# Optimization experiments

Hardware: AMD Instinct MI355X
Metric: run time of the kernel (lower is better)

## Reference

```python
import jax, jax.numpy as jnp
import numpy as np

RES = 128
RANK = 8
PE_L = 6
ENC = 256
N = 1 << 20
IN_DIM = RANK + 3 + 3 * 2 * PE_L  # 47


def _linear_init(key, fan_in, fan_out):
    kw, kb = jax.random.split(key)
    bound = 1.0 / np.sqrt(fan_in)
    W = jax.random.uniform(kw, (fan_in, fan_out), jnp.float32, -bound, bound)
    b = jax.random.uniform(kb, (fan_out,), jnp.float32, -bound, bound)
    return W, b


def setup_inputs() -> dict:
    key = jax.random.key(0)
    ks = jax.random.split(key, 12)
    x = jax.random.uniform(ks[0], (N, 3), jnp.float32, -1.0, 1.0)
    f_xy = jax.random.normal(ks[1], (RANK, RES, RES), jnp.float32)
    f_xz = jax.random.normal(ks[2], (RANK, RES, RES), jnp.float32)
    f_yz = jax.random.normal(ks[3], (RANK, RES, RES), jnp.float32)
    W0, b0 = _linear_init(ks[4], IN_DIM, ENC)
    W1, b1 = _linear_init(ks[5], ENC, ENC)
    W2, b2 = _linear_init(ks[6], ENC, ENC)
    W3, b3 = _linear_init(ks[7], ENC, ENC)
    W_sig, b_sig = _linear_init(ks[8], ENC, 1)
    W_rgb, b_rgb = _linear_init(ks[9], ENC, 3)
    return {
        "x": x, "f_xy": f_xy, "f_xz": f_xz, "f_yz": f_yz,
        "W0": W0, "b0": b0, "W1": W1, "b1": b1,
        "W2": W2, "b2": b2, "W3": W3, "b3": b3,
        "W_sig": W_sig, "b_sig": b_sig, "W_rgb": W_rgb, "b_rgb": b_rgb,
    }


def reference(x, f_xy, f_xz, f_yz, W0, b0, W1, b1, W2, b2, W3, b3,
              W_sig, b_sig, W_rgb, b_rgb):
    # map [-1,1] coords to voxel indices (truncation like .long(), then clamp)
    coords = (x + 1.0) * 0.5 * (RES - 1)
    idx = jnp.clip(coords.astype(jnp.int32), 0, RES - 1)
    ix, iy, iz = idx[:, 0], idx[:, 1], idx[:, 2]
    # tri-planar CP-factor gathers: each [rank, N]
    feat = (f_xy[:, iy, ix] + f_xz[:, iz, ix] + f_yz[:, iz, iy]).T  # [N, rank]
    # positional encoding: [x, (sin(2^l x), cos(2^l x)) for l in 0..L-1]
    freqs = 2.0 ** jnp.arange(PE_L, dtype=jnp.float32)          # [L]
    ang = x[:, None, :] * freqs[None, :, None]                   # [N, L, 3]
    pe_sc = jnp.concatenate([jnp.sin(ang), jnp.cos(ang)], axis=-1)  # [N, L, 6]
    pe = jnp.concatenate([x, pe_sc.reshape(x.shape[0], -1)], axis=-1)  # [N, 3+6L]
    h = jnp.concatenate([feat, pe], axis=-1)                     # [N, 47]
    for W, b in ((W0, b0), (W1, b1), (W2, b2), (W3, b3)):
        h = jax.nn.relu(h @ W + b)
    sigma = jax.nn.softplus(h @ W_sig + b_sig)                   # [N, 1]
    rgb = jax.nn.sigmoid(h @ W_rgb + b_rgb)                      # [N, 3]
    return (rgb, sigma)
```

## Files before the change

kernel.cpp:

```cpp
#include <hip/hip_runtime.h>
#include <hip/hip_bf16.h>

typedef unsigned short ushort_t;
typedef unsigned int uint_t;
typedef unsigned char uchar_t;

typedef float f32x4 __attribute__((ext_vector_type(4)));
typedef float f32x16 __attribute__((ext_vector_type(16)));
typedef int v8i __attribute__((ext_vector_type(8)));

#define NPTS (1 << 20)

#define OFF_FLAG 0
#define OFF_B0   16
#define OFF_B1   272
#define OFF_B2   528
#define OFF_B3   784
#define OFF_BSIG 1040
#define OFF_BRGB 1041
#define OFF_W0   1056
#define OFF_W1   9248
#define OFF_W2   42016
#define OFF_W3   74784
#define OFF_WH   107552
#define OFF_PL   111648

__device__ __forceinline__ float bf2f(ushort_t u) {
  union { uint_t i; float f; } c; c.i = ((uint_t)u) << 16; return c.f;
}
__device__ __forceinline__ ushort_t f2bf(float f) {
  union { float f; uint_t i; } c; c.f = f;
  uint_t x = c.i;
  return (ushort_t)((x + 0x7fffu + ((x >> 16) & 1u)) >> 16);
}
__device__ __forceinline__ uint_t f2fp8b_soft(float x) {
  union { float f; uint_t u; } v; v.f = x;
  uint_t s = (v.u >> 24) & 0x80u;
  float ax = fabsf(x);
  if (ax < 0.015625f) return s | (uint_t)(int)rintf(ax * 512.0f);
  if (ax >= 448.0f) return s | 0x7Eu;
  int e2; float m = frexpf(ax, &e2);
  int q = (int)rintf(m * 16.0f) - 8;
  int e = e2 - 1;
  if (q == 8) { q = 0; ++e; }
  if (e == 8 && q > 6) q = 6;
  return s | ((uint_t)(e + 7) << 3) | (uint_t)q;
}

#if defined(__has_builtin)
#if __has_builtin(__builtin_amdgcn_cvt_pk_fp8_f32)
#define HAVE_HW_FP8 1
#endif
#if __has_builtin(__builtin_amdgcn_mfma_scale_f32_32x32x64_f8f6f4)
#define HAVE_MX 1
#endif
#endif

#ifdef HAVE_HW_FP8
__device__ __forceinline__ uint_t pk4fp8(float a, float b, float c, float d) {
  uint_t r = (uint_t)__builtin_amdgcn_cvt_pk_fp8_f32(a, b, 0, false);
  r = (uint_t)__builtin_amdgcn_cvt_pk_fp8_f32(c, d, r, true);
  return r;
}
__device__ __forceinline__ uchar_t f2fp8(float x) {
  return (uchar_t)(__builtin_amdgcn_cvt_pk_fp8_f32(x, 0.0f, 0, false) & 0xFFu);
}
#else
__device__ __forceinline__ uint_t pk4fp8(float a, float b, float c, float d) {
  return f2fp8b_soft(a) | (f2fp8b_soft(b) << 8) | (f2fp8b_soft(c) << 16) | (f2fp8b_soft(d) << 24);
}
__device__ __forceinline__ uchar_t f2fp8(float x) { return (uchar_t)f2fp8b_soft(x); }
#endif

union AU { v8i v; uint2 u2[4]; long l[4]; };

__device__ __forceinline__ f32x16 mx_mfma(const AU& A, const AU& B, f32x16 C) {
#ifdef HAVE_MX
  return __builtin_amdgcn_mfma_scale_f32_32x32x64_f8f6f4(
      A.v, B.v, C, 0, 0, 0, (int)0x7F7F7F7F, 0, (int)0x7F7F7F7F);
#else
#pragma unroll
  for (int s = 0; s < 4; ++s)
    C = __builtin_amdgcn_mfma_f32_32x32x16_fp8_fp8(A.l[s], B.l[s], C, 0, 0, 0);
  return C;
#endif
}

__device__ __forceinline__ float ldf(const void* p, long i, int isbf) {
  return isbf ? bf2f(((const ushort_t*)p)[i]) : ((const float*)p)[i];
}
__device__ __forceinline__ ushort_t ldbf(const void* p, long i, int isbf) {
  return isbf ? ((const ushort_t*)p)[i] : f2bf(((const float*)p)[i]);
}
__device__ __forceinline__ void stf(void* p, long i, int isbf, float v) {
  if (isbf) ((ushort_t*)p)[i] = f2bf(v);
  else      ((float*)p)[i] = v;
}

__device__ __forceinline__ int fp8addr(int p, int k) {
  return ((p >> 5) << 13) + ((k >> 4) << 9) + (((k >> 3) & 1) << 8)
       + ((p & 31) << 3) + (k & 7);
}

__global__ void sniff_dtype(const void* __restrict__ f, ushort_t* __restrict__ ws) {
  __shared__ int s_cnt;
  if (threadIdx.x == 0) s_cnt = 0;
  __syncthreads();
  const ushort_t* u = (const ushort_t*)f;
  int c = 0;
  for (int j = 0; j < 4; ++j) {
    ushort_t v = u[(threadIdx.x * 4 + j) * 2];
    int e = (v >> 7) & 0xFF;
    if (e > 100 && e < 140) ++c;
  }
  atomicAdd(&s_cnt, c);
  __syncthreads();
  if (threadIdx.x == 0) ((uint_t*)ws)[0] = (s_cnt >= 160) ? 1u : 0u;
}

__global__ void prep_bias(const void* __restrict__ b0, const void* __restrict__ b1,
                          const void* __restrict__ b2, const void* __restrict__ b3,
                          const void* __restrict__ bsig, const void* __restrict__ brgb,
                          ushort_t* __restrict__ ws) {
  const int isbf = (int)((const uint_t*)ws)[0];
  int i = threadIdx.x;
  ws[OFF_B0 + i] = ldbf(b0, i, isbf);
  ws[OFF_B1 + i] = ldbf(b1, i, isbf);
  ws[OFF_B2 + i] = ldbf(b2, i, isbf);
  ws[OFF_B3 + i] = ldbf(b3, i, isbf);
  if (i == 0) ws[OFF_BSIG] = ldbf(bsig, 0, isbf);
  if (i < 3) ws[OFF_BRGB + i] = ldbf(brgb, i, isbf);
}

__global__ void prep_weights(const void* __restrict__ W0,
                             const void* __restrict__ W1,
                             const void* __restrict__ W2,
                             const void* __restrict__ W3,
                             const void* __restrict__ Wsig,
                             const void* __restrict__ Wrgb,
                             ushort_t* __restrict__ ws) {
  const int isbf = (int)((const uint_t*)ws)[0];
  int t = blockIdx.x * 256 + threadIdx.x;
  if (t >= 432 * 64) return;
  int lane = t & 63;
  int tile = t >> 6;
  const void* src = nullptr;
  ushort_t* dst;
  int local, Ksrc = 256;
  bool head = false;
  if (tile < 32) { local = tile; src = W0; Ksrc = 47; dst = ws + OFF_W0 + (size_t)local * 256; }
  else if (tile < 160) { local = tile - 32;  src = W1; dst = ws + OFF_W1 + (size_t)local * 256; }
  else if (tile < 288) { local = tile - 160; src = W2; dst = ws + OFF_W2 + (size_t)local * 256; }
  else if (tile < 416) { local = tile - 288; src = W3; dst = ws + OFF_W3 + (size_t)local * 256; }
  else { local = tile - 416; head = true; dst = ws + OFF_WH + (size_t)local * 256; }
  int kt = head ? local : (local >> 3);
  int mt = head ? 0 : (local & 7);
  int n = mt * 32 + (lane & 31);
  int kb = kt * 16 + (lane >> 5) * 8;
  for (int j = 0; j < 8; j += 4) {
    float v[4];
    for (int jj = 0; jj < 4; ++jj) {
      int k = kb + j + jj;
      float vv = 0.0f;
      if (head) {
        if (n < 3) vv = ldf(Wrgb, (long)k * 3 + n, isbf);
        else if (n == 3) vv = ldf(Wsig, k, isbf);
      } else if (k < Ksrc) {
        vv = ldf(src, (long)k * 256 + n, isbf);
      }
      v[jj] = vv * 16.0f;
    }
    uint_t pk = pk4fp8(v[0], v[1], v[2], v[3]);
    dst[lane * 4 + (j >> 1)]     = (ushort_t)(pk & 0xFFFFu);
    dst[lane * 4 + (j >> 1) + 1] = (ushort_t)(pk >> 16);
  }
}

__global__ void prep_planes(const void* __restrict__ fxy,
                            const void* __restrict__ fxz,
                            const void* __restrict__ fyz,
                            ushort_t* __restrict__ ws) {
  const int isbf = (int)((const uint_t*)ws)[0];
  int t = blockIdx.x * 256 + threadIdx.x;
  int plane = t >> 14, pos = t & 16383;
  const void* src = (plane == 0) ? fxy : (plane == 1) ? fxz : fyz;
  ushort_t* d = ws + OFF_PL + (size_t)plane * 131072 + (size_t)pos * 8;
  for (int r = 0; r < 8; ++r) d[r] = ldbf(src, (long)r * 16384 + pos, isbf);
}

template <int KT, int CUR>
__device__ __forceinline__ void mlp_layer(uchar_t* s_act,
                                          const uchar_t* __restrict__ wsW,
                                          const uchar_t* __restrict__ nextW,
                                          const ushort_t* __restrict__ bias,
                                          int w, int lane, AU (&a)[2][2]) {
  constexpr int G = KT / 4;
  f32x16 acc[2][4] = {};
  const int p31 = lane & 31;
  const int q2 = lane >> 5;
  const uchar_t* bptr = s_act + lane * 8;
  const uchar_t* aptr = wsW + w * 1024 + lane * 8;
  const uchar_t* nptr = nextW + w * 1024 + lane * 8;
  AU b[2];
#pragma unroll
  for (int g = 0; g < G; ++g) {
    const int c = (CUR + g) & 1;
    const uchar_t* ap = (g + 1 < G) ? (aptr + (size_t)(g + 1) * 16384) : nptr;
#pragma unroll
    for (int mi = 0; mi < 2; ++mi)
#pragma unroll
      for (int s = 0; s < 4; ++s)
        a[c ^ 1][mi].u2[s] = *(const uint2*)(ap + s * 4096 + mi * 512);
    const uchar_t* bg = bptr + g * 2048;
#pragma unroll
    for (int s = 0; s < 4; ++s) b[0].u2[s] = *(const uint2*)(bg + s * 512);
#pragma unroll
    for (int d = 0; d < 4; ++d) {
      if (d < 3) {
#pragma unroll
        for (int s = 0; s < 4; ++s)
          b[(d + 1) & 1].u2[s] = *(const uint2*)(bg + (d + 1) * 8192 + s * 512);
      }
      acc[0][d] = mx_mfma(a[c][0], b[d & 1], acc[0][d]);
      acc[1][d] = mx_mfma(a[c][1], b[d & 1], acc[1][d]);
    }
  }
  __syncthreads();
  uchar_t* wbase = s_act + w * 2048 + p31 * 8 + q2 * 4;
#pragma unroll
  for (int mi = 0; mi < 2; ++mi) {
#pragma unroll
    for (int rq = 0; rq < 4; ++rq) {
      int col0 = w * 64 + mi * 32 + rq * 8 + q2 * 4;
      ushort4 bb = *(const ushort4*)(bias + col0);
      float bf0 = bf2f(bb.x), bf1 = bf2f(bb.y), bf2v = bf2f(bb.z), bf3 = bf2f(bb.w);
#pragma unroll
      for (int d = 0; d < 4; ++d) {
        const f32x16& A = acc[mi][d];
        float v0 = fmaxf(fmaf(A[rq * 4 + 0], 0.0625f, bf0), 0.0f);
        float v1 = fmaxf(fmaf(A[rq * 4 + 1], 0.0625f, bf1), 0.0f);
        float v2 = fmaxf(fmaf(A[rq * 4 + 2], 0.0625f, bf2v), 0.0f);
        float v3 = fmaxf(fmaf(A[rq * 4 + 3], 0.0625f, bf3), 0.0f);
        *(uint_t*)(wbase + d * 8192 + mi * 1024 + (rq >> 1) * 512 + (rq & 1) * 256)
            = pk4fp8(v0, v1, v2, v3);
      }
    }
  }
  __syncthreads();
}

__global__ __launch_bounds__(256, 2)
void tensorf_main(const void* __restrict__ x,
                  const ushort_t* __restrict__ ws,
                  void* __restrict__ out) {
  __shared__ uchar_t s_act[4 * 16 * 512];
  const int isbf = (int)((const uint_t*)ws)[0];
  const int tid = threadIdx.x;
  const int lane = tid & 63;
  const int wid = tid >> 6;
  const int blk = blockIdx.x;

  AU a[2][2];
  {
    const uchar_t* a0 = (const uchar_t*)(ws + OFF_W0) + wid * 1024 + lane * 8;
#pragma unroll
    for (int mi = 0; mi < 2; ++mi)
#pragma unroll
      for (int s = 0; s < 4; ++s)
        a[0][mi].u2[s] = *(const uint2*)(a0 + s * 4096 + mi * 512);
  }

  {
    int pl = tid >> 1;
    int s = tid & 1;
    long p = (long)blk * 128 + pl;
    float x0 = ldf(x, p * 3 + 0, isbf);
    float x1 = ldf(x, p * 3 + 1, isbf);
    float x2 = ldf(x, p * 3 + 2, isbf);
    float fx[3] = { x0, x1, x2 };
    if (s == 0) {
      int ix = (int)(((x0 + 1.0f) * 0.5f) * 127.0f);
      int iy = (int)(((x1 + 1.0f) * 0.5f) * 127.0f);
      int iz = (int)(((x2 + 1.0f) * 0.5f) * 127.0f);
      ix = ix < 0 ? 0 : (ix > 127 ? 127 : ix);
      iy = iy < 0 ? 0 : (iy > 127 ? 127 : iy);
      iz = iz < 0 ? 0 : (iz > 127 ? 127 : iz);
      union { uint4 u; ushort_t s[8]; } a4, b4, c4;
      a4.u = *(const uint4*)(ws + OFF_PL + (size_t)(iy * 128 + ix) * 8);
      b4.u = *(const uint4*)(ws + OFF_PL + 131072 + (size_t)(iz * 128 + ix) * 8);
      c4.u = *(const uint4*)(ws + OFF_PL + 262144 + (size_t)(iz * 128 + iy) * 8);
      float fv[8];
#pragma unroll
      for (int r = 0; r < 8; ++r)
        fv[r] = bf2f(a4.s[r]) + bf2f(b4.s[r]) + bf2f(c4.s[r]);
      uint2 f;
      f.x = pk4fp8(fv[0], fv[1], fv[2], fv[3]);
      f.y = pk4fp8(fv[4], fv[5], fv[6], fv[7]);
      *(uint2*)(s_act + fp8addr(pl, 0)) = f;
      s_act[fp8addr(pl, 8)]  = f2fp8(x0);
      s_act[fp8addr(pl, 9)]  = f2fp8(x1);
      s_act[fp8addr(pl, 10)] = f2fp8(x2);
#pragma unroll
      for (int l = 4; l < 6; ++l) {
        float fr = (float)(1 << l);
        int k0 = 11 + l * 6;
#pragma unroll
        for (int dd = 0; dd < 3; ++dd) {
          float ang = fx[dd] * fr;
          s_act[fp8addr(pl, k0 + dd)]     = f2fp8(__sinf(ang));
          s_act[fp8addr(pl, k0 + 3 + dd)] = f2fp8(__cosf(ang));
        }
      }
      s_act[fp8addr(pl, 47)] = 0;
      *(uint2*)(s_act + fp8addr(pl, 48)) = uint2{0u, 0u};
      *(uint2*)(s_act + fp8addr(pl, 56)) = uint2{0u, 0u};
    } else {
#pragma unroll
      for (int l = 0; l < 4; ++l) {
        float fr = (float)(1 << l);
        int k0 = 11 + l * 6;
#pragma unroll
        for (int dd = 0; dd < 3; ++dd) {
          float ang = fx[dd] * fr;
          s_act[fp8addr(pl, k0 + dd)]     = f2fp8(__sinf(ang));
          s_act[fp8addr(pl, k0 + 3 + dd)] = f2fp8(__cosf(ang));
        }
      }
    }
  }
  __syncthreads();

  const uchar_t* w0 = (const uchar_t*)(ws + OFF_W0);
  const uchar_t* w1 = (const uchar_t*)(ws + OFF_W1);
  const uchar_t* w2 = (const uchar_t*)(ws + OFF_W2);
  const uchar_t* w3 = (const uchar_t*)(ws + OFF_W3);
  const uchar_t* wh = (const uchar_t*)(ws + OFF_WH);
  mlp_layer<4, 0>(s_act,  w0, w1, ws + OFF_B0, wid, lane, a);
  mlp_layer<16, 1>(s_act, w1, w2, ws + OFF_B1, wid, lane, a);
  mlp_layer<16, 1>(s_act, w2, w3, ws + OFF_B2, wid, lane, a);
  mlp_layer<16, 1>(s_act, w3, wh, ws + OFF_B3, wid, lane, a);

  {
    f32x16 acc = {};
    const int p31 = lane & 31;
    const int q2 = lane >> 5;
    const uchar_t* hb = s_act + wid * 8192 + lane * 8;
    const uchar_t* whp = wh + lane * 8;
    AU ta, tb;
#pragma unroll
    for (int g = 0; g < 4; ++g) {
#pragma unroll
      for (int s = 0; s < 4; ++s) {
        ta.u2[s] = *(const uint2*)(whp + (size_t)(4 * g + s) * 512);
        tb.u2[s] = *(const uint2*)(hb + (size_t)(4 * g + s) * 512);
      }
      acc = mx_mfma(ta, tb, acc);
    }
    if (q2 == 0) {
      long pp = (long)blk * 128 + wid * 32 + p31;
      float br0 = bf2f(ws[OFF_BRGB + 0]), br1 = bf2f(ws[OFF_BRGB + 1]), br2 = bf2f(ws[OFF_BRGB + 2]);
      float bs = bf2f(ws[OFF_BSIG]);
      float z0 = fmaf(acc[0], 0.0625f, br0);
      float z1 = fmaf(acc[1], 0.0625f, br1);
      float z2 = fmaf(acc[2], 0.0625f, br2);
      stf(out, pp * 3 + 0, isbf, 1.0f / (1.0f + __expf(-z0)));
      stf(out, pp * 3 + 1, isbf, 1.0f / (1.0f + __expf(-z1)));
      stf(out, pp * 3 + 2, isbf, 1.0f / (1.0f + __expf(-z2)));
      float zs = fmaf(acc[3], 0.0625f, bs);
      float sp = (zs > 20.0f) ? zs : __logf(1.0f + __expf(zs));
      stf(out, (long)3 * NPTS + pp, isbf, sp);
    }
  }
}

extern "C" void kernel_launch(void* const* d_in, const int* in_sizes, int n_in,
                              void* d_out, int out_size, void* d_ws, size_t ws_size,
                              hipStream_t stream) {
  const void* x    = d_in[0];
  const void* fxy  = d_in[1];
  const void* fxz  = d_in[2];
  const void* fyz  = d_in[3];
  const void* W0   = d_in[4];
  const void* b0   = d_in[5];
  const void* W1   = d_in[6];
  const void* b1   = d_in[7];
  const void* W2   = d_in[8];
  const void* b2   = d_in[9];
  const void* W3   = d_in[10];
  const void* b3   = d_in[11];
  const void* Wsig = d_in[12];
  const void* bsig = d_in[13];
  const void* Wrgb = d_in[14];
  const void* brgb = d_in[15];
  ushort_t* ws = (ushort_t*)d_ws;

  hipLaunchKernelGGL(sniff_dtype, dim3(1), dim3(64), 0, stream, fxy, ws);
  hipLaunchKernelGGL(prep_bias, dim3(1), dim3(256), 0, stream,
                     b0, b1, b2, b3, bsig, brgb, ws);
  hipLaunchKernelGGL(prep_weights, dim3(108), dim3(256), 0, stream,
                     W0, W1, W2, W3, Wsig, Wrgb, ws);
  hipLaunchKernelGGL(prep_planes, dim3(192), dim3(256), 0, stream,
                     fxy, fxz, fyz, ws);
  hipLaunchKernelGGL(tensorf_main, dim3(8192), dim3(256), 0, stream,
                     x, ws, d_out);
}
```

Measured before the change: 355.1 us.

## Double-buffer MLP activations in LDS and drop the pre-epilogue barrier

Activations now alternate between two shared-memory buffers across layers, so each layer reads one buffer and writes the other. This removes the __syncthreads between the MFMA loop and the epilogue writes, because a write can no longer overwrite data another wave is still reading. The bias, scale and ReLU epilogue is also rewritten with 2-wide float vectors so the compiler can emit packed FP32 ops. In exchange, LDS use doubles to 64 KB per block, which may reduce occupancy under the 2-blocks-per-CU launch bound.

```diff
diff --git a/kernel.cpp b/kernel.cpp
--- a/kernel.cpp
+++ b/kernel.cpp
@@ -5,6 +5,7 @@
 typedef unsigned int uint_t;
 typedef unsigned char uchar_t;
 
+typedef float f32x2 __attribute__((ext_vector_type(2)));
 typedef float f32x4 __attribute__((ext_vector_type(4)));
 typedef float f32x16 __attribute__((ext_vector_type(16)));
 typedef int v8i __attribute__((ext_vector_type(8)));
@@ -189,7 +190,8 @@
 }
 
 template <int KT, int CUR>
-__device__ __forceinline__ void mlp_layer(uchar_t* s_act,
+__device__ __forceinline__ void mlp_layer(const uchar_t* __restrict__ act_in,
+                                          uchar_t* __restrict__ act_out,
                                           const uchar_t* __restrict__ wsW,
                                           const uchar_t* __restrict__ nextW,
                                           const ushort_t* __restrict__ bias,
@@ -198,7 +200,7 @@
   f32x16 acc[2][4] = {};
   const int p31 = lane & 31;
   const int q2 = lane >> 5;
-  const uchar_t* bptr = s_act + lane * 8;
+  const uchar_t* bptr = act_in + lane * 8;
   const uchar_t* aptr = wsW + w * 1024 + lane * 8;
   const uchar_t* nptr = nextW + w * 1024 + lane * 8;
   AU b[2];
@@ -225,24 +227,28 @@
       acc[1][d] = mx_mfma(a[c][1], b[d & 1], acc[1][d]);
     }
   }
-  __syncthreads();
-  uchar_t* wbase = s_act + w * 2048 + p31 * 8 + q2 * 4;
+  uchar_t* wbase = act_out + w * 2048 + p31 * 8 + q2 * 4;
+  const f32x2 sc2 = { 0.0625f, 0.0625f };
+  const f32x2 zero2 = { 0.0f, 0.0f };
 #pragma unroll
   for (int mi = 0; mi < 2; ++mi) {
 #pragma unroll
     for (int rq = 0; rq < 4; ++rq) {
       int col0 = w * 64 + mi * 32 + rq * 8 + q2 * 4;
       ushort4 bb = *(const ushort4*)(bias + col0);
-      float bf0 = bf2f(bb.x), bf1 = bf2f(bb.y), bf2v = bf2f(bb.z), bf3 = bf2f(bb.w);
+      f32x2 b01 = { bf2f(bb.x), bf2f(bb.y) };
+      f32x2 b23 = { bf2f(bb.z), bf2f(bb.w) };
 #pragma unroll
       for (int d = 0; d < 4; ++d) {
         const f32x16& A = acc[mi][d];
-        float v0 = fmaxf(fmaf(A[rq * 4 + 0], 0.0625f, bf0), 0.0f);
-        float v1 = fmaxf(fmaf(A[rq * 4 + 1], 0.0625f, bf1), 0.0f);
-        float v2 = fmaxf(fmaf(A[rq * 4 + 2], 0.0625f, bf2v), 0.0f);
-        float v3 = fmaxf(fmaf(A[rq * 4 + 3], 0.0625f, bf3), 0.0f);
+        f32x2 z01 = { A[rq * 4 + 0], A[rq * 4 + 1] };
+        f32x2 z23 = { A[rq * 4 + 2], A[rq * 4 + 3] };
+        z01 = z01 * sc2 + b01;
+        z23 = z23 * sc2 + b23;
+        z01 = __builtin_elementwise_max(z01, zero2);
+        z23 = __builtin_elementwise_max(z23, zero2);
         *(uint_t*)(wbase + d * 8192 + mi * 1024 + (rq >> 1) * 512 + (rq & 1) * 256)
-            = pk4fp8(v0, v1, v2, v3);
+            = pk4fp8(z01.x, z01.y, z23.x, z23.y);
       }
     }
   }
@@ -253,7 +259,7 @@
 void tensorf_main(const void* __restrict__ x,
                   const ushort_t* __restrict__ ws,
                   void* __restrict__ out) {
-  __shared__ uchar_t s_act[4 * 16 * 512];
+  __shared__ uchar_t s_act[2][4 * 16 * 512];
   const int isbf = (int)((const uint_t*)ws)[0];
   const int tid = threadIdx.x;
   const int lane = tid & 63;
@@ -271,6 +277,7 @@
   }
 
   {
+    uchar_t* act0 = s_act[0];
     int pl = tid >> 1;
     int s = tid & 1;
     long p = (long)blk * 128 + pl;
@@ -296,10 +303,10 @@
       uint2 f;
       f.x = pk4fp8(fv[0], fv[1], fv[2], fv[3]);
       f.y = pk4fp8(fv[4], fv[5], fv[6], fv[7]);
-      *(uint2*)(s_act + fp8addr(pl, 0)) = f;
-      s_act[fp8addr(pl, 8)]  = f2fp8(x0);
-      s_act[fp8addr(pl, 9)]  = f2fp8(x1);
-      s_act[fp8addr(pl, 10)] = f2fp8(x2);
+      *(uint2*)(act0 + fp8addr(pl, 0)) = f;
+      act0[fp8addr(pl, 8)]  = f2fp8(x0);
+      act0[fp8addr(pl, 9)]  = f2fp8(x1);
+      act0[fp8addr(pl, 10)] = f2fp8(x2);
 #pragma unroll
       for (int l = 4; l < 6; ++l) {
         float fr = (float)(1 << l);
@@ -307,13 +314,13 @@
 #pragma unroll
         for (int dd = 0; dd < 3; ++dd) {
           float ang = fx[dd] * fr;
-          s_act[fp8addr(pl, k0 + dd)]     = f2fp8(__sinf(ang));
-          s_act[fp8addr(pl, k0 + 3 + dd)] = f2fp8(__cosf(ang));
+          act0[fp8addr(pl, k0 + dd)]     = f2fp8(__sinf(ang));
+          act0[fp8addr(pl, k0 + 3 + dd)] = f2fp8(__cosf(ang));
         }
       }
-      s_act[fp8addr(pl, 47)] = 0;
-      *(uint2*)(s_act + fp8addr(pl, 48)) = uint2{0u, 0u};
-      *(uint2*)(s_act + fp8addr(pl, 56)) = uint2{0u, 0u};
+      act0[fp8addr(pl, 47)] = 0;
+      *(uint2*)(act0 + fp8addr(pl, 48)) = uint2{0u, 0u};
+      *(uint2*)(act0 + fp8addr(pl, 56)) = uint2{0u, 0u};
     } else {
 #pragma unroll
       for (int l = 0; l < 4; ++l) {
@@ -322,8 +329,8 @@
 #pragma unroll
         for (int dd = 0; dd < 3; ++dd) {
           float ang = fx[dd] * fr;
-          s_act[fp8addr(pl, k0 + dd)]     = f2fp8(__sinf(ang));
-          s_act[fp8addr(pl, k0 + 3 + dd)] = f2fp8(__cosf(ang));
+          act0[fp8addr(pl, k0 + dd)]     = f2fp8(__sinf(ang));
+          act0[fp8addr(pl, k0 + 3 + dd)] = f2fp8(__cosf(ang));
         }
       }
     }
@@ -335,16 +342,16 @@
   const uchar_t* w2 = (const uchar_t*)(ws + OFF_W2);
   const uchar_t* w3 = (const uchar_t*)(ws + OFF_W3);
   const uchar_t* wh = (const uchar_t*)(ws + OFF_WH);
-  mlp_layer<4, 0>(s_act,  w0, w1, ws + OFF_B0, wid, lane, a);
-  mlp_layer<16, 1>(s_act, w1, w2, ws + OFF_B1, wid, lane, a);
-  mlp_layer<16, 1>(s_act, w2, w3, ws + OFF_B2, wid, lane, a);
-  mlp_layer<16, 1>(s_act, w3, wh, ws + OFF_B3, wid, lane, a);
+  mlp_layer<4, 0>(s_act[0], s_act[1],  w0, w1, ws + OFF_B0, wid, lane, a);
+  mlp_layer<16, 1>(s_act[1], s_act[0], w1, w2, ws + OFF_B1, wid, lane, a);
+  mlp_layer<16, 1>(s_act[0], s_act[1], w2, w3, ws + OFF_B2, wid, lane, a);
+  mlp_layer<16, 1>(s_act[1], s_act[0], w3, wh, ws + OFF_B3, wid, lane, a);
 
   {
     f32x16 acc = {};
     const int p31 = lane & 31;
     const int q2 = lane >> 5;
-    const uchar_t* hb = s_act + wid * 8192 + lane * 8;
+    const uchar_t* hb = s_act[0] + wid * 8192 + lane * 8;
     const uchar_t* whp = wh + lane * 8;
     AU ta, tb;
 #pragma unroll
```

Measured after the change: 358.6 us. No clear change (+1.0%).
